# Performance work log

Hardware: AMD Instinct MI355X
Metric: run time of the kernel (lower is better)

The kernel has to match this reference:

```python
import jax, jax.numpy as jnp
import numpy as np

NUM_HEADS = 16
NUM_KV_HEADS = 4
HEAD_DIM = 128
ROPE_BASE = 10000.0


def _rotate_half(x):
    half = x.shape[-1] // 2
    return jnp.concatenate([-x[..., half:], x[..., :half]], axis=-1)


def _rope_cos_sin(seq_len, dim, dtype):
    inv_freq = 1.0 / (ROPE_BASE ** (jnp.arange(0, dim, 2, dtype=jnp.float32) / dim))
    t = jnp.arange(seq_len, dtype=jnp.float32)
    freqs = jnp.outer(t, inv_freq)            # (T, dim/2)
    emb = jnp.concatenate([freqs, freqs], -1)  # (T, dim)
    return jnp.cos(emb).astype(dtype), jnp.sin(emb).astype(dtype)


def setup_inputs() -> dict:
    key = jax.random.key(0)
    ks = jax.random.split(key, 5)
    B, T, D = 2, 2048, 2048
    Dkv = NUM_KV_HEADS * HEAD_DIM
    s = 1.0 / np.sqrt(D)
    return {
        "x": jax.random.normal(ks[0], (B, T, D), jnp.float32),
        "Wq": jax.random.normal(ks[1], (D, D), jnp.float32) * s,
        "Wk": jax.random.normal(ks[2], (D, Dkv), jnp.float32) * s,
        "Wv": jax.random.normal(ks[3], (D, Dkv), jnp.float32) * s,
        "Wo": jax.random.normal(ks[4], (D, D), jnp.float32) * s,
    }


def reference(x, Wq, Wk, Wv, Wo):
    B, T, D = x.shape
    H, Hkv, hd = NUM_HEADS, NUM_KV_HEADS, HEAD_DIM
    # projections, split heads -> (B, H, T, hd)
    q = (x @ Wq).reshape(B, T, H, hd).transpose(0, 2, 1, 3)
    k = (x @ Wk).reshape(B, T, Hkv, hd).transpose(0, 2, 1, 3)
    v = (x @ Wv).reshape(B, T, Hkv, hd).transpose(0, 2, 1, 3)
    # RoPE on q and k
    cos, sin = _rope_cos_sin(T, hd, x.dtype)  # (T, hd) each
    q = q * cos + _rotate_half(q) * sin
    k = k * cos + _rotate_half(k) * sin
    # GQA: repeat_interleave KV heads to match Q heads
    r = H // Hkv
    k = jnp.repeat(k, r, axis=1)
    v = jnp.repeat(v, r, axis=1)
    # causal SDPA
    scale = hd ** -0.5
    scores = jnp.einsum('bhqd,bhkd->bhqk', q, k) * scale
    causal = jnp.tril(jnp.ones((T, T), bool))
    scores = jnp.where(causal, scores, jnp.finfo(scores.dtype).min)
    attn = jax.nn.softmax(scores, axis=-1)
    out = jnp.einsum('bhqk,bhkd->bhqd', attn, v)
    out = out.transpose(0, 2, 1, 3).reshape(B, T, D)
    return out @ Wo
```

## Files before the change

kernel.cpp:

```cpp
#include <hip/hip_runtime.h>

typedef __bf16 bf16x8 __attribute__((ext_vector_type(8)));
typedef float floatx4 __attribute__((ext_vector_type(4)));
typedef unsigned short ushort_t;
typedef ushort_t ushortx4 __attribute__((ext_vector_type(4)));
typedef float floatx4v __attribute__((ext_vector_type(4)));

typedef __attribute__((address_space(1))) void gvoid;
typedef __attribute__((address_space(3))) void svoid;

#define MFMA16(a, b, c) __builtin_amdgcn_mfma_f32_16x16x32_bf16(a, b, c, 0, 0, 0)

__device__ __forceinline__ ushort_t f2bf(float f) {
  unsigned u = __builtin_bit_cast(unsigned, f);
  u += 0x7fffu + ((u >> 16) & 1u);
  return (ushort_t)(u >> 16);
}

__device__ __forceinline__ void gld16(const ushort_t* g, ushort_t* l) {
  __builtin_amdgcn_global_load_lds((gvoid*)(g), (svoid*)(l), 16, 0, 0);
}

__global__ __launch_bounds__(256) void k_prep(const floatx4v* __restrict__ xin,
                                              ushortx4* __restrict__ x_bf,
                                              const float* __restrict__ Wq,
                                              const float* __restrict__ Wk,
                                              const float* __restrict__ Wv,
                                              const float* __restrict__ Wo,
                                              ushort_t* __restrict__ WqkvT,
                                              ushort_t* __restrict__ WoT) {
  __shared__ float tile[64][65];
  if (blockIdx.x < 8192) {
    int i = blockIdx.x * 256 + threadIdx.x;
    floatx4v v = xin[i];
    ushortx4 o;
    o[0] = f2bf(v[0]); o[1] = f2bf(v[1]); o[2] = f2bf(v[2]); o[3] = f2bf(v[3]);
    x_bf[i] = o;
    return;
  }
  const int pb = blockIdx.x - 8192;
  const int byy = pb / 80;
  const int bx = pb - byy * 80;
  const float* in;
  ushort_t* out;
  int N, cx;
  if (bx < 32)      { in = Wq; out = WqkvT;              N = 2048; cx = bx; }
  else if (bx < 40) { in = Wk; out = WqkvT + 2048*2048;  N = 512;  cx = bx - 32; }
  else if (bx < 48) { in = Wv; out = WqkvT + 2560*2048;  N = 512;  cx = bx - 40; }
  else              { in = Wo; out = WoT;                N = 2048; cx = bx - 48; }
  const int c0 = cx * 64;
  const int k0 = byy * 64;
  const int tx = threadIdx.x & 63;
  const int ty = threadIdx.x >> 6;
#pragma unroll
  for (int i = 0; i < 16; i++) {
    int row = i * 4 + ty;
    tile[tx][row] = in[(k0 + row) * N + c0 + tx];
  }
  __syncthreads();
#pragma unroll
  for (int i = 0; i < 16; i++) {
    int nr = i * 4 + ty;
    out[(c0 + nr) * 2048 + k0 + tx] = f2bf(tile[nr][tx]);
  }
}

__global__ __launch_bounds__(256, 3) void k_gemm_qkv(const ushort_t* __restrict__ A,
                                                     const ushort_t* __restrict__ Bt,
                                                     ushort_t* __restrict__ Qh,
                                                     ushort_t* __restrict__ Kh,
                                                     ushort_t* __restrict__ Vt) {
  __shared__ __align__(16) ushort_t As[2][4096];
  __shared__ __align__(16) ushort_t Bs[2][4096];
  const int t = threadIdx.x;
  const int w = t >> 6;
  const int lane = t & 63;
  const int r = lane & 15;
  const int q = lane >> 4;
  const int m0 = blockIdx.y * 128;
  const int n0 = blockIdx.x * 128;

  const int srow = t >> 2;
  const int gc = (t & 3) ^ ((t >> 3) & 3);
  const int a_g0 = (m0 + srow) * 2048 + gc * 8;
  const int b_g0 = (n0 + srow) * 2048 + gc * 8;

  const int pos8 = (q ^ ((r >> 1) & 3)) * 8;
  const int a_off = (w * 32 + r) * 32 + pos8;
  const int b_off = r * 32 + pos8;

  const floatx4 fz = {0.f, 0.f, 0.f, 0.f};
  floatx4 acc[2][8];
#pragma unroll
  for (int i = 0; i < 2; i++)
#pragma unroll
    for (int jj = 0; jj < 8; jj++) acc[i][jj] = fz;

  gld16(A + a_g0, As[0] + t * 8);
  gld16(A + a_g0 + 64 * 2048, As[0] + 2048 + t * 8);
  gld16(Bt + b_g0, Bs[0] + t * 8);
  gld16(Bt + b_g0 + 64 * 2048, Bs[0] + 2048 + t * 8);

  for (int it = 0; it < 64; it++) {
    const int c = it & 1;
    __syncthreads();
    if (it < 63) {
      const int kt = (it + 1) * 32;
      gld16(A + a_g0 + kt, As[1 - c] + t * 8);
      gld16(A + a_g0 + 64 * 2048 + kt, As[1 - c] + 2048 + t * 8);
      gld16(Bt + b_g0 + kt, Bs[1 - c] + t * 8);
      gld16(Bt + b_g0 + 64 * 2048 + kt, Bs[1 - c] + 2048 + t * 8);
    }
    bf16x8 af0 = *(const bf16x8*)(As[c] + a_off);
    bf16x8 af1 = *(const bf16x8*)(As[c] + a_off + 512);
    bf16x8 bfv[8];
#pragma unroll
    for (int ni = 0; ni < 8; ni++) bfv[ni] = *(const bf16x8*)(Bs[c] + b_off + ni * 512);
#pragma unroll
    for (int ni = 0; ni < 8; ni++) {
      acc[0][ni] = MFMA16(af0, bfv[ni], acc[0][ni]);
      acc[1][ni] = MFMA16(af1, bfv[ni], acc[1][ni]);
    }
  }

  const int bb = m0 >> 11;
  const int trow0 = (m0 & 2047) + w * 32;

  if (n0 < 2560) {
    const bool isQ = (n0 < 2048);
    const float scale = isQ ? 0.08838834764831845f : 1.0f;
    ushort_t* dst = isQ ? (Qh + ((bb * 16 + (n0 >> 7)) * 2048) * 128)
                        : (Kh + ((bb * 4 + ((n0 - 2048) >> 7)) * 2048) * 128);
#pragma unroll
    for (int mi = 0; mi < 2; mi++) {
#pragma unroll
      for (int ni = 0; ni < 4; ni++) {
        const int d = ni * 16 + r;
        const float invf = __expf(-0.14391156643f * (float)d);
#pragma unroll
        for (int reg = 0; reg < 4; reg++) {
          const int tt = trow0 + mi * 16 + q * 4 + reg;
          float sn, cs;
          __sincosf((float)tt * invf, &sn, &cs);
          const float lo = acc[mi][ni][reg];
          const float hi = acc[mi][ni + 4][reg];
          dst[tt * 128 + d] = f2bf((lo * cs - hi * sn) * scale);
          dst[tt * 128 + d + 64] = f2bf((hi * cs + lo * sn) * scale);
        }
      }
    }
  } else {
    ushort_t* dst = Vt + ((bb * 4 + ((n0 - 2560) >> 7)) * 128) * 2048;
#pragma unroll
    for (int mi = 0; mi < 2; mi++) {
#pragma unroll
      for (int ni = 0; ni < 8; ni++) {
        const int d = ni * 16 + r;
        const int t0 = trow0 + mi * 16 + q * 4;
        ushortx4 pk;
#pragma unroll
        for (int reg = 0; reg < 4; reg++) pk[reg] = f2bf(acc[mi][ni][reg]);
        *(ushortx4*)(dst + d * 2048 + t0) = pk;
      }
    }
  }
}

__global__ __launch_bounds__(256) void k_flash(const ushort_t* __restrict__ Qh,
                                               const ushort_t* __restrict__ Kh,
                                               const ushort_t* __restrict__ Vt,
                                               ushort_t* __restrict__ attn) {
  __shared__ __align__(16) ushort_t smem[36864];

  const int t = threadIdx.x;
  const int w = t >> 6;
  const int lane = t & 63;
  const int r = lane & 15;
  const int q = lane >> 4;
  const int rx = r & 7;

  const int xcd = blockIdx.x & 7;
  const int s_ = blockIdx.x >> 3;
  const int bh2 = s_ & 3;
  const int st = s_ >> 2;
  const int ti = 31 - st;
  const int bh = xcd * 4 + bh2;
  const int jmax = ti + 1;

  const int b = bh >> 4;
  const int h = bh & 15;
  const int hkv = h >> 2;

  const ushort_t* Qg = Qh + (bh * 2048) * 128;
  const ushort_t* Kg = Kh + ((b * 4 + hkv) * 2048) * 128;
  const ushort_t* Vg = Vt + ((b * 4 + hkv) * 128) * 2048;
  ushort_t* Pw = smem + 32768 + w * 1024;

  {
    const int qrow = t >> 4;
    const int gcq = (t & 15) ^ (qrow & 7);
#pragma unroll
    for (int i = 0; i < 4; i++)
      gld16(Qg + (ti * 64 + i * 16 + qrow) * 128 + gcq * 8, smem + i * 2048 + t * 8);
  }
  __syncthreads();
  bf16x8 aq[4];
#pragma unroll
  for (int ks = 0; ks < 4; ks++) {
    const int pp = ((ks * 4 + q) ^ rx) * 8;
    aq[ks] = *(const bf16x8*)(smem + (w * 16 + r) * 128 + pp);
  }
  __syncthreads();

  const int krow = t >> 4;
  const int gck = (t & 15) ^ (krow & 7);
  const int vrow = t >> 3;
  const int gcv = (t & 7) ^ (vrow & 7);

#pragma unroll
  for (int i = 0; i < 4; i++)
    gld16(Kg + (i * 16 + krow) * 128 + gck * 8, smem + i * 2048 + t * 8);
#pragma unroll
  for (int i = 0; i < 4; i++)
    gld16(Vg + (i * 32 + vrow) * 2048 + gcv * 8, smem + 16384 + i * 2048 + t * 8);

  const floatx4 fz = {0.f, 0.f, 0.f, 0.f};
  floatx4 acc[8];
#pragma unroll
  for (int nd = 0; nd < 8; nd++) acc[nd] = fz;
  float lsum[4];
#pragma unroll
  for (int reg = 0; reg < 4; reg++) lsum[reg] = 0.f;

  for (int j = 0; j < jmax; j++) {
    const int c = j & 1;
    const ushort_t* Kc = smem + c * 8192;
    const ushort_t* Vc = smem + 16384 + c * 8192;
    __syncthreads();
    if (j + 1 < jmax) {
      ushort_t* Kn = smem + (1 - c) * 8192;
      ushort_t* Vn = smem + 16384 + (1 - c) * 8192;
#pragma unroll
      for (int i = 0; i < 4; i++)
        gld16(Kg + ((j + 1) * 64 + i * 16 + krow) * 128 + gck * 8, Kn + i * 2048 + t * 8);
#pragma unroll
      for (int i = 0; i < 4; i++)
        gld16(Vg + (i * 32 + vrow) * 2048 + (j + 1) * 64 + gcv * 8, Vn + i * 2048 + t * 8);
    }

    floatx4 s[4];
#pragma unroll
    for (int ni = 0; ni < 4; ni++) s[ni] = fz;
#pragma unroll
    for (int ks = 0; ks < 4; ks++) {
      const int pp = ((ks * 4 + q) ^ rx) * 8;
#pragma unroll
      for (int ni = 0; ni < 4; ni++) {
        bf16x8 bk = *(const bf16x8*)(Kc + (ni * 16 + r) * 128 + pp);
        s[ni] = MFMA16(aq[ks], bk, s[ni]);
      }
    }
    if (j == jmax - 1) {
#pragma unroll
      for (int ni = 0; ni < 4; ni++)
#pragma unroll
        for (int reg = 0; reg < 4; reg++) {
          const int row_l = w * 16 + q * 4 + reg;
          const int col_l = ni * 16 + r;
          if (col_l > row_l) s[ni][reg] = -1e30f;
        }
    }
#pragma unroll
    for (int ni = 0; ni < 4; ni++)
#pragma unroll
      for (int reg = 0; reg < 4; reg++)
        s[ni][reg] = __expf(s[ni][reg] - 8.0f);
#pragma unroll
    for (int reg = 0; reg < 4; reg++)
      lsum[reg] += (s[0][reg] + s[1][reg]) + (s[2][reg] + s[3][reg]);
#pragma unroll
    for (int ni = 0; ni < 4; ni++)
#pragma unroll
      for (int reg = 0; reg < 4; reg++) {
        const int lr = q * 4 + reg;
        const int col = ni * 16 + r;
        Pw[lr * 64 + ((col >> 3) ^ (lr & 7)) * 8 + (col & 7)] = f2bf(s[ni][reg]);
      }
#pragma unroll
    for (int ks = 0; ks < 2; ks++) {
      const int pp = ((ks * 4 + q) ^ rx) * 8;
      bf16x8 ap = *(const bf16x8*)(Pw + r * 64 + pp);
#pragma unroll
      for (int nd = 0; nd < 8; nd++) {
        bf16x8 bv = *(const bf16x8*)(Vc + (nd * 16 + r) * 64 + pp);
        acc[nd] = MFMA16(ap, bv, acc[nd]);
      }
    }
  }

#pragma unroll
  for (int reg = 0; reg < 4; reg++) {
#pragma unroll
    for (int d = 1; d < 16; d <<= 1)
      lsum[reg] += __shfl_xor(lsum[reg], d);
  }
  ushort_t* dst = attn + (b * 2048 + ti * 64) * 2048 + h * 128;
#pragma unroll
  for (int reg = 0; reg < 4; reg++) {
    const int row_l = w * 16 + q * 4 + reg;
    const float inv = 1.0f / lsum[reg];
#pragma unroll
    for (int nd = 0; nd < 8; nd++)
      dst[row_l * 2048 + nd * 16 + r] = f2bf(acc[nd][reg] * inv);
  }
}

__global__ __launch_bounds__(256) void k_gemm_out(const ushort_t* __restrict__ A,
                                                  const ushort_t* __restrict__ Bt,
                                                  float* __restrict__ out) {
  __shared__ __align__(16) ushort_t As[2][4096];
  __shared__ __align__(16) ushort_t Bs[2][4096];
  const int t = threadIdx.x;
  const int w = t >> 6;
  const int lane = t & 63;
  const int r = lane & 15;
  const int q = lane >> 4;
  const int m0 = blockIdx.y * 128;
  const int n0 = blockIdx.x * 128;

  const int srow = t >> 2;
  const int gc = (t & 3) ^ ((t >> 3) & 3);
  const int a_g0 = (m0 + srow) * 2048 + gc * 8;
  const int b_g0 = (n0 + srow) * 2048 + gc * 8;

  const int pos8 = (q ^ ((r >> 1) & 3)) * 8;
  const int a_off = (w * 32 + r) * 32 + pos8;
  const int b_off = r * 32 + pos8;

  const floatx4 fz = {0.f, 0.f, 0.f, 0.f};
  floatx4 acc[2][8];
#pragma unroll
  for (int i = 0; i < 2; i++)
#pragma unroll
    for (int jj = 0; jj < 8; jj++) acc[i][jj] = fz;

  gld16(A + a_g0, As[0] + t * 8);
  gld16(A + a_g0 + 64 * 2048, As[0] + 2048 + t * 8);
  gld16(Bt + b_g0, Bs[0] + t * 8);
  gld16(Bt + b_g0 + 64 * 2048, Bs[0] + 2048 + t * 8);

  for (int it = 0; it < 64; it++) {
    const int c = it & 1;
    __syncthreads();
    if (it < 63) {
      const int kt = (it + 1) * 32;
      gld16(A + a_g0 + kt, As[1 - c] + t * 8);
      gld16(A + a_g0 + 64 * 2048 + kt, As[1 - c] + 2048 + t * 8);
      gld16(Bt + b_g0 + kt, Bs[1 - c] + t * 8);
      gld16(Bt + b_g0 + 64 * 2048 + kt, Bs[1 - c] + 2048 + t * 8);
    }
    bf16x8 af0 = *(const bf16x8*)(As[c] + a_off);
    bf16x8 af1 = *(const bf16x8*)(As[c] + a_off + 512);
    bf16x8 bfv[8];
#pragma unroll
    for (int ni = 0; ni < 8; ni++) bfv[ni] = *(const bf16x8*)(Bs[c] + b_off + ni * 512);
#pragma unroll
    for (int ni = 0; ni < 8; ni++) {
      acc[0][ni] = MFMA16(af0, bfv[ni], acc[0][ni]);
      acc[1][ni] = MFMA16(af1, bfv[ni], acc[1][ni]);
    }
  }

#pragma unroll
  for (int mi = 0; mi < 2; mi++)
#pragma unroll
    for (int ni = 0; ni < 8; ni++)
#pragma unroll
      for (int reg = 0; reg < 4; reg++)
        out[(m0 + w * 32 + mi * 16 + q * 4 + reg) * 2048 + n0 + ni * 16 + r] =
            acc[mi][ni][reg];
}

extern "C" void kernel_launch(void* const* d_in, const int* in_sizes, int n_in,
                              void* d_out, int out_size, void* d_ws, size_t ws_size,
                              hipStream_t stream) {
  (void)in_sizes; (void)n_in; (void)out_size; (void)ws_size;
  const float* x  = (const float*)d_in[0];
  const float* Wq = (const float*)d_in[1];
  const float* Wk = (const float*)d_in[2];
  const float* Wv = (const float*)d_in[3];
  const float* Wo = (const float*)d_in[4];
  float* out = (float*)d_out;

  char* ws = (char*)d_ws;
  ushort_t* x_bf   = (ushort_t*)(ws);
  ushort_t* WqkvT  = (ushort_t*)(ws + 16777216);
  ushort_t* WoT    = (ushort_t*)(ws + 29360128);
  ushort_t* Qh     = (ushort_t*)(ws + 37748736);
  ushort_t* Kh     = (ushort_t*)(ws + 54525952);
  ushort_t* Vt     = (ushort_t*)(ws + 58720256);
  ushort_t* attn   = (ushort_t*)(ws + 62914560);

  k_prep<<<8192 + 2560, 256, 0, stream>>>((const floatx4v*)x, (ushortx4*)x_bf,
                                          Wq, Wk, Wv, Wo, WqkvT, WoT);
  k_gemm_qkv<<<dim3(24, 32), 256, 0, stream>>>(x_bf, WqkvT, Qh, Kh, Vt);
  k_flash<<<1024, 256, 0, stream>>>(Qh, Kh, Vt, attn);
  k_gemm_out<<<dim3(16, 32), 256, 0, stream>>>(attn, WoT, out);
}
```

Before: 284.4 us.

## Restructure QKV GEMM into 256x256 tiles with 8 waves and staged prefetch

The QKV projection GEMM moves from 128x128 tiles with 4 waves and K-step 32 to 256x256 tiles with 8 waves, K-step 64 and a 1D grid of 192 blocks. Each block maps to its tile through a swizzled index. The k-loop splits into four quadrant MFMA phases, and each phase issues one quarter of the next tile's global-to-LDS loads, with explicit vmcnt waits, barriers and setprio. The aim is more operand reuse per byte loaded and global loads hidden behind MFMA work. In exchange, 192 blocks is fewer than the CU count, so occupancy drops, and register and LDS pressure is high (128 KB LDS per block).

```diff
diff --git a/kernel.cpp b/kernel.cpp
--- a/kernel.cpp
+++ b/kernel.cpp
@@ -65,102 +65,209 @@
   }
 }
 
-__global__ __launch_bounds__(256, 3) void k_gemm_qkv(const ushort_t* __restrict__ A,
+__global__ __launch_bounds__(512, 2) void k_gemm_qkv(const ushort_t* __restrict__ A,
                                                      const ushort_t* __restrict__ Bt,
                                                      ushort_t* __restrict__ Qh,
                                                      ushort_t* __restrict__ Kh,
                                                      ushort_t* __restrict__ Vt) {
-  __shared__ __align__(16) ushort_t As[2][4096];
-  __shared__ __align__(16) ushort_t Bs[2][4096];
-  const int t = threadIdx.x;
-  const int w = t >> 6;
-  const int lane = t & 63;
+  __shared__ __align__(16) ushort_t smem[65536];
+
+  const int tid = threadIdx.x;
+  const int lane = tid & 63;
+  const int w = tid >> 6;
+  const int wm = w >> 2;
+  const int wn = w & 3;
   const int r = lane & 15;
   const int q = lane >> 4;
-  const int m0 = blockIdx.y * 128;
-  const int n0 = blockIdx.x * 128;
-
-  const int srow = t >> 2;
-  const int gc = (t & 3) ^ ((t >> 3) & 3);
-  const int a_g0 = (m0 + srow) * 2048 + gc * 8;
-  const int b_g0 = (n0 + srow) * 2048 + gc * 8;
-
-  const int pos8 = (q ^ ((r >> 1) & 3)) * 8;
-  const int a_off = (w * 32 + r) * 32 + pos8;
-  const int b_off = r * 32 + pos8;
+  const int rx7 = r & 7;
+
+  const int bid = blockIdx.x;
+  const int s = bid >> 3;
+  const int mhi = (s >= 12) ? 1 : 0;
+  const int n_t = s - mhi * 12;
+  const int m_t = (bid & 7) * 2 + mhi;
+  const int m0 = m_t * 256;
+  const int n0 = n_t * 256;
+
+  const int srow = tid >> 3;
+  const int sch = tid & 7;
+  const int scol = (sch ^ (srow & 7)) * 8;
+  const ushort_t* Ag = A + (m0 + srow) * 2048 + scol;
+  const ushort_t* Bg = Bt + (n0 + srow) * 2048 + scol;
+
+#define STG_A(bufc, half, kk) do {                                                        \
+    gld16(Ag + ((half) * 128) * 2048 + (kk),                                              \
+          smem + (bufc) * 16384 + ((half) * 128 + srow) * 64 + sch * 8);                  \
+    gld16(Ag + ((half) * 128 + 64) * 2048 + (kk),                                         \
+          smem + (bufc) * 16384 + ((half) * 128 + 64 + srow) * 64 + sch * 8);             \
+  } while (0)
+#define STG_B(bufc, half, kk) do {                                                        \
+    gld16(Bg + ((half) * 128) * 2048 + (kk),                                              \
+          smem + 32768 + (bufc) * 16384 + ((half) * 128 + srow) * 64 + sch * 8);          \
+    gld16(Bg + ((half) * 128 + 64) * 2048 + (kk),                                         \
+          smem + 32768 + (bufc) * 16384 + ((half) * 128 + 64 + srow) * 64 + sch * 8);     \
+  } while (0)
+
+  const int arow = wm * 16 + r;
+  const int brow = wn * 16 + r;
+  const int ch0 = (q ^ rx7) * 8;
+  const int ch1 = ((4 + q) ^ rx7) * 8;
 
   const floatx4 fz = {0.f, 0.f, 0.f, 0.f};
-  floatx4 acc[2][8];
-#pragma unroll
-  for (int i = 0; i < 2; i++)
-#pragma unroll
-    for (int jj = 0; jj < 8; jj++) acc[i][jj] = fz;
-
-  gld16(A + a_g0, As[0] + t * 8);
-  gld16(A + a_g0 + 64 * 2048, As[0] + 2048 + t * 8);
-  gld16(Bt + b_g0, Bs[0] + t * 8);
-  gld16(Bt + b_g0 + 64 * 2048, Bs[0] + 2048 + t * 8);
-
-  for (int it = 0; it < 64; it++) {
-    const int c = it & 1;
-    __syncthreads();
-    if (it < 63) {
-      const int kt = (it + 1) * 32;
-      gld16(A + a_g0 + kt, As[1 - c] + t * 8);
-      gld16(A + a_g0 + 64 * 2048 + kt, As[1 - c] + 2048 + t * 8);
-      gld16(Bt + b_g0 + kt, Bs[1 - c] + t * 8);
-      gld16(Bt + b_g0 + 64 * 2048 + kt, Bs[1 - c] + 2048 + t * 8);
-    }
-    bf16x8 af0 = *(const bf16x8*)(As[c] + a_off);
-    bf16x8 af1 = *(const bf16x8*)(As[c] + a_off + 512);
-    bf16x8 bfv[8];
-#pragma unroll
-    for (int ni = 0; ni < 8; ni++) bfv[ni] = *(const bf16x8*)(Bs[c] + b_off + ni * 512);
-#pragma unroll
-    for (int ni = 0; ni < 8; ni++) {
-      acc[0][ni] = MFMA16(af0, bfv[ni], acc[0][ni]);
-      acc[1][ni] = MFMA16(af1, bfv[ni], acc[1][ni]);
-    }
-  }
+  floatx4 acc[8][4];
+#pragma unroll
+  for (int i = 0; i < 8; i++)
+#pragma unroll
+    for (int j = 0; j < 4; j++) acc[i][j] = fz;
+
+  STG_A(0, 0, 0); STG_B(0, 0, 0); STG_B(0, 1, 0); STG_A(0, 1, 0);
+
+  for (int t = 0; t < 32; ++t) {
+    const int c = t & 1;
+    const int nc = 1 - c;
+    const ushort_t* Ac = smem + c * 16384;
+    const ushort_t* Bc = smem + 32768 + c * 16384;
+    const bool st = (t + 1 < 32);
+    const int kt1 = (t + 1) * 64;
+
+    bf16x8 a0f[4][2], a1f[4][2], b0f[2][2], b1f[2][2];
+
+    asm volatile("s_waitcnt vmcnt(4)" ::: "memory");
+    asm volatile("s_barrier" ::: "memory");
+#pragma unroll
+    for (int mf = 0; mf < 4; mf++) {
+      const ushort_t* ap = Ac + (mf * 32 + arow) * 64;
+      a0f[mf][0] = *(const bf16x8*)(ap + ch0);
+      a0f[mf][1] = *(const bf16x8*)(ap + ch1);
+    }
+#pragma unroll
+    for (int nq = 0; nq < 2; nq++) {
+      const ushort_t* bp = Bc + (nq * 64 + brow) * 64;
+      b0f[nq][0] = *(const bf16x8*)(bp + ch0);
+      b0f[nq][1] = *(const bf16x8*)(bp + ch1);
+    }
+    if (st) STG_A(nc, 0, kt1);
+    __builtin_amdgcn_s_setprio(1);
+#pragma unroll
+    for (int ks = 0; ks < 2; ks++)
+#pragma unroll
+      for (int mf = 0; mf < 4; mf++)
+#pragma unroll
+        for (int nq = 0; nq < 2; nq++)
+          acc[mf][nq] = MFMA16(a0f[mf][ks], b0f[nq][ks], acc[mf][nq]);
+    __builtin_amdgcn_s_setprio(0);
+
+    if (st) { asm volatile("s_waitcnt vmcnt(4)" ::: "memory"); }
+    else    { asm volatile("s_waitcnt vmcnt(2)" ::: "memory"); }
+    asm volatile("s_barrier" ::: "memory");
+#pragma unroll
+    for (int nq = 0; nq < 2; nq++) {
+      const ushort_t* bp = Bc + (128 + nq * 64 + brow) * 64;
+      b1f[nq][0] = *(const bf16x8*)(bp + ch0);
+      b1f[nq][1] = *(const bf16x8*)(bp + ch1);
+    }
+    if (st) STG_B(nc, 0, kt1);
+    __builtin_amdgcn_s_setprio(1);
+#pragma unroll
+    for (int ks = 0; ks < 2; ks++)
+#pragma unroll
+      for (int mf = 0; mf < 4; mf++)
+#pragma unroll
+        for (int nq = 0; nq < 2; nq++)
+          acc[mf][2 + nq] = MFMA16(a0f[mf][ks], b1f[nq][ks], acc[mf][2 + nq]);
+    __builtin_amdgcn_s_setprio(0);
+
+    if (st) { asm volatile("s_waitcnt vmcnt(4)" ::: "memory"); }
+    else    { asm volatile("s_waitcnt vmcnt(0)" ::: "memory"); }
+    asm volatile("s_barrier" ::: "memory");
+#pragma unroll
+    for (int mf = 0; mf < 4; mf++) {
+      const ushort_t* ap = Ac + (128 + mf * 32 + arow) * 64;
+      a1f[mf][0] = *(const bf16x8*)(ap + ch0);
+      a1f[mf][1] = *(const bf16x8*)(ap + ch1);
+    }
+    if (st) STG_B(nc, 1, kt1);
+    __builtin_amdgcn_s_setprio(1);
+#pragma unroll
+    for (int ks = 0; ks < 2; ks++)
+#pragma unroll
+      for (int mf = 0; mf < 4; mf++)
+#pragma unroll
+        for (int nq = 0; nq < 2; nq++)
+          acc[4 + mf][2 + nq] = MFMA16(a1f[mf][ks], b1f[nq][ks], acc[4 + mf][2 + nq]);
+    __builtin_amdgcn_s_setprio(0);
+
+    if (st) STG_A(nc, 1, kt1);
+    __builtin_amdgcn_s_setprio(1);
+#pragma unroll
+    for (int ks = 0; ks < 2; ks++)
+#pragma unroll
+      for (int mf = 0; mf < 4; mf++)
+#pragma unroll
+        for (int nq = 0; nq < 2; nq++)
+          acc[4 + mf][nq] = MFMA16(a1f[mf][ks], b0f[nq][ks], acc[4 + mf][nq]);
+    __builtin_amdgcn_s_setprio(0);
+  }
+#undef STG_A
+#undef STG_B
 
   const int bb = m0 >> 11;
-  const int trow0 = (m0 & 2047) + w * 32;
-
-  if (n0 < 2560) {
-    const bool isQ = (n0 < 2048);
-    const float scale = isQ ? 0.08838834764831845f : 1.0f;
-    ushort_t* dst = isQ ? (Qh + ((bb * 16 + (n0 >> 7)) * 2048) * 128)
-                        : (Kh + ((bb * 4 + ((n0 - 2048) >> 7)) * 2048) * 128);
-#pragma unroll
-    for (int mi = 0; mi < 2; mi++) {
-#pragma unroll
-      for (int ni = 0; ni < 4; ni++) {
-        const int d = ni * 16 + r;
-        const float invf = __expf(-0.14391156643f * (float)d);
+  const int tbase = (m0 & 2047) + wm * 16;
+
+  if (n0 < 2048) {
+    const float scale = 0.08838834764831845f;
+    const int d = wn * 16 + r;
+    const float invf = __expf(-0.14391156643f * (float)d);
+#pragma unroll
+    for (int pr = 0; pr < 2; pr++) {
+      ushort_t* dst = Qh + ((bb * 16 + (n0 >> 7) + pr) * 2048) * 128;
+#pragma unroll
+      for (int mf = 0; mf < 8; mf++)
 #pragma unroll
         for (int reg = 0; reg < 4; reg++) {
-          const int tt = trow0 + mi * 16 + q * 4 + reg;
+          const int tt = tbase + mf * 32 + q * 4 + reg;
           float sn, cs;
           __sincosf((float)tt * invf, &sn, &cs);
-          const float lo = acc[mi][ni][reg];
-          const float hi = acc[mi][ni + 4][reg];
+          const float lo = acc[mf][2 * pr][reg];
+          const float hi = acc[mf][2 * pr + 1][reg];
           dst[tt * 128 + d] = f2bf((lo * cs - hi * sn) * scale);
           dst[tt * 128 + d + 64] = f2bf((hi * cs + lo * sn) * scale);
         }
-      }
+    }
+  } else if (n0 < 2560) {
+    const int d = wn * 16 + r;
+    const float invf = __expf(-0.14391156643f * (float)d);
+#pragma unroll
+    for (int pr = 0; pr < 2; pr++) {
+      ushort_t* dst = Kh + ((bb * 4 + ((n0 - 2048) >> 7) + pr) * 2048) * 128;
+#pragma unroll
+      for (int mf = 0; mf < 8; mf++)
+#pragma unroll
+        for (int reg = 0; reg < 4; reg++) {
+          const int tt = tbase + mf * 32 + q * 4 + reg;
+          float sn, cs;
+          __sincosf((float)tt * invf, &sn, &cs);
+          const float lo = acc[mf][2 * pr][reg];
+          const float hi = acc[mf][2 * pr + 1][reg];
+          dst[tt * 128 + d] = f2bf(lo * cs - hi * sn);
+          dst[tt * 128 + d + 64] = f2bf(hi * cs + lo * sn);
+        }
     }
   } else {
-    ushort_t* dst = Vt + ((bb * 4 + ((n0 - 2560) >> 7)) * 128) * 2048;
-#pragma unroll
-    for (int mi = 0; mi < 2; mi++) {
-#pragma unroll
-      for (int ni = 0; ni < 8; ni++) {
-        const int d = ni * 16 + r;
-        const int t0 = trow0 + mi * 16 + q * 4;
-        ushortx4 pk;
-#pragma unroll
-        for (int reg = 0; reg < 4; reg++) pk[reg] = f2bf(acc[mi][ni][reg]);
-        *(ushortx4*)(dst + d * 2048 + t0) = pk;
+#pragma unroll
+    for (int pr = 0; pr < 2; pr++) {
+      ushort_t* dst = Vt + ((bb * 4 + ((n0 - 2560) >> 7) + pr) * 128) * 2048;
+#pragma unroll
+      for (int nq = 0; nq < 2; nq++) {
+        const int d = nq * 64 + wn * 16 + r;
+#pragma unroll
+        for (int mf = 0; mf < 8; mf++) {
+          const int t0 = tbase + mf * 32 + q * 4;
+          ushortx4 pk;
+#pragma unroll
+          for (int reg = 0; reg < 4; reg++) pk[reg] = f2bf(acc[mf][2 * pr + nq][reg]);
+          *(ushortx4*)(dst + d * 2048 + t0) = pk;
+        }
       }
     }
   }
@@ -403,7 +510,7 @@
 
   k_prep<<<8192 + 2560, 256, 0, stream>>>((const floatx4v*)x, (ushortx4*)x_bf,
                                           Wq, Wk, Wv, Wo, WqkvT, WoT);
-  k_gemm_qkv<<<dim3(24, 32), 256, 0, stream>>>(x_bf, WqkvT, Qh, Kh, Vt);
+  k_gemm_qkv<<<192, 512, 0, stream>>>(x_bf, WqkvT, Qh, Kh, Vt);
   k_flash<<<1024, 256, 0, stream>>>(Qh, Kh, Vt, attn);
   k_gemm_out<<<dim3(16, 32), 256, 0, stream>>>(attn, WoT, out);
 }
```

After: 280.6 us. Within noise of the previous version (-1.4%).
